# Optimization experiments

Measured on AMD Instinct MI355X. Metric: run time of the kernel, lower is better.

Reference implementation:

```python
import jax, jax.numpy as jnp
import numpy as np

EPS = 1e-06

def _feature_map(x):
    # elu_feature_map: phi(x) = elu(x) + 1  (strictly positive features)
    return jax.nn.elu(x) + 1.0

def setup_inputs() -> dict:
    key = jax.random.key(0)
    kq, kk, kv = jax.random.split(key, 3)
    N, L, H, D, M = 2, 2048, 8, 64, 64
    return {
        "queries": jax.random.normal(kq, (N, L, H, D), dtype=jnp.float32),
        "keys": jax.random.normal(kk, (N, L, H, D), dtype=jnp.float32),
        "values": jax.random.normal(kv, (N, L, H, M), dtype=jnp.float32),
    }

def reference(queries, keys, values):
    Q = _feature_map(queries)   # [N,L,H,D]
    K = _feature_map(keys)      # [N,L,H,D]
    # normalizer: Z_i = 1 / (Q_i . sum_{j<=i} K_j + eps)
    Z = 1.0 / (jnp.einsum('nlhi,nlhi->nlh', Q, jnp.cumsum(K, axis=1)) + EPS)
    # causal linear attention: S_i = sum_{j<=i} K_j outer V_j ; out_i = Q_i @ S_i
    S = jnp.cumsum(jnp.einsum('nlhd,nlhm->nlhdm', K, values), axis=1)  # [N,L,H,D,M]
    V = jnp.einsum('nlhd,nlhdm->nlhm', Q, S)
    return V * Z[:, :, :, None]
```

## Files before the change

### kernel.cpp

```cpp
#include <hip/hip_runtime.h>


namespace {
constexpr int N_ = 2, L_ = 2048, H_ = 8, D_ = 64, M_ = 64;
constexpr int C  = 64;
constexpr int G  = L_ / C;
constexpr int NH = N_ * H_;
constexpr int LDH = H_ * D_;
constexpr int TS  = 72;
constexpr float EPS_ = 1e-6f;
}

typedef __attribute__((ext_vector_type(8))) short short8;
typedef __attribute__((ext_vector_type(4))) float f32x4;

__device__ __forceinline__ float phi(float x) {
    return x > 0.0f ? x + 1.0f : __expf(x);
}
__device__ __forceinline__ unsigned short f2bf(float x) {
    unsigned int u = __float_as_uint(x);
    u += 0x7fffu + ((u >> 16) & 1u);
    return (unsigned short)(u >> 16);
}
__device__ __forceinline__ float bf2f(unsigned short h) {
    return __uint_as_float(((unsigned int)h) << 16);
}

__global__ __launch_bounds__(256, 4) void k_chunksum(
    const float* __restrict__ keys, const float* __restrict__ values,
    float* __restrict__ wsS, float* __restrict__ wsK)
{
    __shared__ __align__(16) unsigned short Kt[C * TS];
    __shared__ __align__(16) unsigned short Vt[C * TS];
    const int bid = blockIdx.x;
    const int g = bid % G, nh = bid / G;
    const int n = nh / H_, h = nh % H_;
    const int t = threadIdx.x;
    const size_t base = ((size_t)(n * L_ + g * C) * H_ + h) * D_;

#pragma unroll
    for (int r = 0; r < 4; ++r) {
        const int f = t + 256 * r;
        const int j = f >> 4, c = (f & 15) * 4;
        const size_t ga = base + (size_t)j * LDH + c;
        const float4 kv = *(const float4*)(keys + ga);
        const float4 vv = *(const float4*)(values + ga);
        Kt[(c + 0) * TS + j] = f2bf(phi(kv.x));
        Kt[(c + 1) * TS + j] = f2bf(phi(kv.y));
        Kt[(c + 2) * TS + j] = f2bf(phi(kv.z));
        Kt[(c + 3) * TS + j] = f2bf(phi(kv.w));
        Vt[(c + 0) * TS + j] = f2bf(vv.x);
        Vt[(c + 1) * TS + j] = f2bf(vv.y);
        Vt[(c + 2) * TS + j] = f2bf(vv.z);
        Vt[(c + 3) * TS + j] = f2bf(vv.w);
    }
    __syncthreads();

    const int w = t >> 6, lane = t & 63;
    const int row16 = lane & 15, quad = lane >> 4;

    f32x4 acc[4] = {f32x4{0,0,0,0}, f32x4{0,0,0,0}, f32x4{0,0,0,0}, f32x4{0,0,0,0}};
    f32x4 accK = f32x4{0,0,0,0};
    const unsigned short one_bf = 0x3F80;
    short8 ones;
#pragma unroll
    for (int i = 0; i < 8; ++i) ones[i] = (short)one_bf;

#pragma unroll
    for (int kt = 0; kt < 2; ++kt) {
        const short8 a = *(const short8*)&Kt[(16 * w + row16) * TS + quad * 8 + 32 * kt];
#pragma unroll
        for (int c = 0; c < 4; ++c) {
            const short8 b = *(const short8*)&Vt[(16 * c + row16) * TS + quad * 8 + 32 * kt];
            acc[c] = __builtin_amdgcn_mfma_f32_16x16x32_bf16(a, b, acc[c], 0, 0, 0);
        }
        accK = __builtin_amdgcn_mfma_f32_16x16x32_bf16(a, ones, accK, 0, 0, 0);
    }

    float* Sc = wsS + (size_t)bid * (D_ * M_);
#pragma unroll
    for (int c = 0; c < 4; ++c)
#pragma unroll
        for (int r = 0; r < 4; ++r)
            Sc[(16 * w + quad * 4 + r) * M_ + 16 * c + row16] = acc[c][r];

    if (row16 == 0) {
#pragma unroll
        for (int r = 0; r < 4; ++r)
            wsK[(size_t)bid * D_ + 16 * w + quad * 4 + r] = accK[r];
    }
}

__global__ __launch_bounds__(256) void k_scan(
    float* __restrict__ wsS, float* __restrict__ wsK)
{
    const int bid = blockIdx.x;
    const int nh = bid >> 4, q = bid & 15;
    const int t = threadIdx.x;

    float* base = wsS + (size_t)nh * G * (D_ * M_) + q * 256 + t;
    float run = 0.f;
#pragma unroll
    for (int g = 0; g < G; ++g) {
        float* p = base + (size_t)g * (D_ * M_);
        const float v = *p;
        *p = run;
        run += v;
    }

    if (q == 0 && t < D_) {
        float rk = 0.f;
        float* kb = wsK + (size_t)nh * G * D_ + t;
#pragma unroll
        for (int g = 0; g < G; ++g) {
            float* p = kb + (size_t)g * D_;
            const float v = *p;
            *p = rk;
            rk += v;
        }
    }
}

__global__ __launch_bounds__(256, 4) void k_out(
    const float* __restrict__ queries, const float* __restrict__ keys,
    const float* __restrict__ values, float* __restrict__ out,
    const float* __restrict__ wsS, const float* __restrict__ wsK)
{
    __shared__ __align__(16) unsigned short Qb[C * TS];
    __shared__ __align__(16) unsigned short Kb[C * TS];
    __shared__ __align__(16) unsigned short Vt[C * TS];
    __shared__ __align__(16) unsigned short St[C * TS];
    __shared__ float Rs[C];
    __shared__ float Zs[C];

    const int bid = blockIdx.x;
    const int g = bid % G, nh = bid / G;
    const int n = nh / H_, h = nh % H_;
    const int t = threadIdx.x;
    const size_t base = ((size_t)(n * L_ + g * C) * H_ + h) * D_;
    const float* Sp = wsS + (size_t)bid * (D_ * M_);
    const float* kpref = wsK + (size_t)bid * D_;

#pragma unroll
    for (int r = 0; r < 4; ++r) {
        const int f = t + 256 * r;
        const int row = f >> 4, c = (f & 15) * 4;
        const size_t ga = base + (size_t)row * LDH + c;
        const float4 qv = *(const float4*)(queries + ga);
        const float4 kv = *(const float4*)(keys + ga);
        const float4 vv = *(const float4*)(values + ga);
        Qb[row * TS + c + 0] = f2bf(phi(qv.x));
        Qb[row * TS + c + 1] = f2bf(phi(qv.y));
        Qb[row * TS + c + 2] = f2bf(phi(qv.z));
        Qb[row * TS + c + 3] = f2bf(phi(qv.w));
        Kb[row * TS + c + 0] = f2bf(phi(kv.x));
        Kb[row * TS + c + 1] = f2bf(phi(kv.y));
        Kb[row * TS + c + 2] = f2bf(phi(kv.z));
        Kb[row * TS + c + 3] = f2bf(phi(kv.w));
        Vt[(c + 0) * TS + row] = f2bf(vv.x);
        Vt[(c + 1) * TS + row] = f2bf(vv.y);
        Vt[(c + 2) * TS + row] = f2bf(vv.z);
        Vt[(c + 3) * TS + row] = f2bf(vv.w);
        const float4 sv = *(const float4*)(Sp + (size_t)row * M_ + c);
        St[(c + 0) * TS + row] = f2bf(sv.x);
        St[(c + 1) * TS + row] = f2bf(sv.y);
        St[(c + 2) * TS + row] = f2bf(sv.z);
        St[(c + 3) * TS + row] = f2bf(sv.w);
    }
    __syncthreads();

    const int w = t >> 6, lane = t & 63;
    const int row16 = lane & 15, quad = lane >> 4;

    short8 aq[2];
#pragma unroll
    for (int kt = 0; kt < 2; ++kt)
        aq[kt] = *(const short8*)&Qb[(16 * w + row16) * TS + quad * 8 + 32 * kt];

    f32x4 accA[4] = {f32x4{0,0,0,0}, f32x4{0,0,0,0}, f32x4{0,0,0,0}, f32x4{0,0,0,0}};
#pragma unroll
    for (int kt = 0; kt < 2; ++kt)
#pragma unroll
        for (int c = 0; c < 4; ++c) {
            const short8 b = *(const short8*)&Kb[(16 * c + row16) * TS + quad * 8 + 32 * kt];
            accA[c] = __builtin_amdgcn_mfma_f32_16x16x32_bf16(aq[kt], b, accA[c], 0, 0, 0);
        }

    float rs[4] = {0.f, 0.f, 0.f, 0.f};
#pragma unroll
    for (int c = 0; c < 4; ++c)
#pragma unroll
        for (int r = 0; r < 4; ++r) {
            const int row = 16 * w + quad * 4 + r;
            const int col = 16 * c + row16;
            const float v = (col <= row) ? accA[c][r] : 0.f;
            accA[c][r] = v;
            rs[r] += v;
        }
#pragma unroll
    for (int off = 1; off < 16; off <<= 1)
#pragma unroll
        for (int r = 0; r < 4; ++r)
            rs[r] += __shfl_xor(rs[r], off, 64);
    if (row16 == 0) {
#pragma unroll
        for (int r = 0; r < 4; ++r)
            Rs[16 * w + quad * 4 + r] = rs[r];
    }
    __syncthreads();

#pragma unroll
    for (int c = 0; c < 4; ++c)
#pragma unroll
        for (int r = 0; r < 4; ++r)
            Kb[(16 * w + quad * 4 + r) * TS + 16 * c + row16] = f2bf(accA[c][r]);

    if (t < C) {
        float zd = 0.f;
#pragma unroll 8
        for (int d = 0; d < D_; ++d)
            zd += bf2f(Qb[t * TS + d]) * kpref[d];
        Zs[t] = 1.0f / (zd + Rs[t] + EPS_);
    }
    __syncthreads();

    f32x4 accO[4] = {f32x4{0,0,0,0}, f32x4{0,0,0,0}, f32x4{0,0,0,0}, f32x4{0,0,0,0}};
#pragma unroll
    for (int kt = 0; kt < 2; ++kt) {
        const short8 aA = *(const short8*)&Kb[(16 * w + row16) * TS + quad * 8 + 32 * kt];
#pragma unroll
        for (int c = 0; c < 4; ++c) {
            const short8 bV = *(const short8*)&Vt[(16 * c + row16) * TS + quad * 8 + 32 * kt];
            accO[c] = __builtin_amdgcn_mfma_f32_16x16x32_bf16(aA, bV, accO[c], 0, 0, 0);
        }
#pragma unroll
        for (int c = 0; c < 4; ++c) {
            const short8 bS = *(const short8*)&St[(16 * c + row16) * TS + quad * 8 + 32 * kt];
            accO[c] = __builtin_amdgcn_mfma_f32_16x16x32_bf16(aq[kt], bS, accO[c], 0, 0, 0);
        }
    }

#pragma unroll
    for (int r = 0; r < 4; ++r) {
        const int row = 16 * w + quad * 4 + r;
        const float z = Zs[row];
        const size_t ob = ((size_t)(n * L_ + g * C + row) * H_ + h) * M_;
#pragma unroll
        for (int c = 0; c < 4; ++c)
            out[ob + 16 * c + row16] = accO[c][r] * z;
    }
}

extern "C" void kernel_launch(void* const* d_in, const int* in_sizes, int n_in,
                              void* d_out, int out_size, void* d_ws, size_t ws_size,
                              hipStream_t stream) {
    const float* q = (const float*)d_in[0];
    const float* k = (const float*)d_in[1];
    const float* v = (const float*)d_in[2];
    float* out = (float*)d_out;
    float* wsS = (float*)d_ws;
    float* wsK = wsS + (size_t)NH * G * D_ * M_;

    k_chunksum<<<dim3(NH * G), dim3(256), 0, stream>>>(k, v, wsS, wsK);
    k_scan<<<dim3(NH * 16), dim3(256), 0, stream>>>(wsS, wsK);
    k_out<<<dim3(NH * G), dim3(256), 0, stream>>>(q, k, v, out, wsS, wsK);
}
```

Before: 86.02 us.

## Store chunk state workspace as transposed bf16 to cut memory traffic

After: 84.67 us. No clear change (-1.6%).

```diff
diff --git a/kernel.cpp b/kernel.cpp
--- a/kernel.cpp
+++ b/kernel.cpp
@@ -28,7 +28,7 @@
 
 __global__ __launch_bounds__(256, 4) void k_chunksum(
     const float* __restrict__ keys, const float* __restrict__ values,
-    float* __restrict__ wsS, float* __restrict__ wsK)
+    unsigned short* __restrict__ wsSb, float* __restrict__ wsK)
 {
     __shared__ __align__(16) unsigned short Kt[C * TS];
     __shared__ __align__(16) unsigned short Vt[C * TS];
@@ -61,10 +61,9 @@
 
     f32x4 acc[4] = {f32x4{0,0,0,0}, f32x4{0,0,0,0}, f32x4{0,0,0,0}, f32x4{0,0,0,0}};
     f32x4 accK = f32x4{0,0,0,0};
-    const unsigned short one_bf = 0x3F80;
     short8 ones;
 #pragma unroll
-    for (int i = 0; i < 8; ++i) ones[i] = (short)one_bf;
+    for (int i = 0; i < 8; ++i) ones[i] = (short)0x3F80;
 
 #pragma unroll
     for (int kt = 0; kt < 2; ++kt) {
@@ -77,12 +76,14 @@
         accK = __builtin_amdgcn_mfma_f32_16x16x32_bf16(a, ones, accK, 0, 0, 0);
     }
 
-    float* Sc = wsS + (size_t)bid * (D_ * M_);
-#pragma unroll
-    for (int c = 0; c < 4; ++c)
-#pragma unroll
-        for (int r = 0; r < 4; ++r)
-            Sc[(16 * w + quad * 4 + r) * M_ + 16 * c + row16] = acc[c][r];
+    unsigned short* Sc = wsSb + (size_t)bid * (D_ * M_);
+#pragma unroll
+    for (int c = 0; c < 4; ++c) {
+        ushort4 pk;
+        pk.x = f2bf(acc[c][0]); pk.y = f2bf(acc[c][1]);
+        pk.z = f2bf(acc[c][2]); pk.w = f2bf(acc[c][3]);
+        *(ushort4*)(Sc + (16 * c + row16) * D_ + 16 * w + quad * 4) = pk;
+    }
 
     if (row16 == 0) {
 #pragma unroll
@@ -92,20 +93,23 @@
 }
 
 __global__ __launch_bounds__(256) void k_scan(
-    float* __restrict__ wsS, float* __restrict__ wsK)
+    unsigned short* __restrict__ wsSb, float* __restrict__ wsK)
 {
     const int bid = blockIdx.x;
-    const int nh = bid >> 4, q = bid & 15;
+    const int nh = bid >> 3, q = bid & 7;
     const int t = threadIdx.x;
 
-    float* base = wsS + (size_t)nh * G * (D_ * M_) + q * 256 + t;
-    float run = 0.f;
+    unsigned int* base =
+        (unsigned int*)(wsSb + (size_t)nh * G * (D_ * M_) + q * 512 + t * 2);
+    float r0 = 0.f, r1 = 0.f;
 #pragma unroll
     for (int g = 0; g < G; ++g) {
-        float* p = base + (size_t)g * (D_ * M_);
-        const float v = *p;
-        *p = run;
-        run += v;
+        unsigned int* p = base + (size_t)g * (D_ * M_ / 2);
+        const unsigned int v = *p;
+        const float v0 = bf2f((unsigned short)(v & 0xffffu));
+        const float v1 = bf2f((unsigned short)(v >> 16));
+        *p = ((unsigned int)f2bf(r1) << 16) | (unsigned int)f2bf(r0);
+        r0 += v0; r1 += v1;
     }
 
     if (q == 0 && t < D_) {
@@ -124,7 +128,7 @@
 __global__ __launch_bounds__(256, 4) void k_out(
     const float* __restrict__ queries, const float* __restrict__ keys,
     const float* __restrict__ values, float* __restrict__ out,
-    const float* __restrict__ wsS, const float* __restrict__ wsK)
+    const unsigned short* __restrict__ wsSb, const float* __restrict__ wsK)
 {
     __shared__ __align__(16) unsigned short Qb[C * TS];
     __shared__ __align__(16) unsigned short Kb[C * TS];
@@ -138,7 +142,7 @@
     const int n = nh / H_, h = nh % H_;
     const int t = threadIdx.x;
     const size_t base = ((size_t)(n * L_ + g * C) * H_ + h) * D_;
-    const float* Sp = wsS + (size_t)bid * (D_ * M_);
+    const unsigned short* Spb = wsSb + (size_t)bid * (D_ * M_);
     const float* kpref = wsK + (size_t)bid * D_;
 
 #pragma unroll
@@ -161,11 +165,12 @@
         Vt[(c + 1) * TS + row] = f2bf(vv.y);
         Vt[(c + 2) * TS + row] = f2bf(vv.z);
         Vt[(c + 3) * TS + row] = f2bf(vv.w);
-        const float4 sv = *(const float4*)(Sp + (size_t)row * M_ + c);
-        St[(c + 0) * TS + row] = f2bf(sv.x);
-        St[(c + 1) * TS + row] = f2bf(sv.y);
-        St[(c + 2) * TS + row] = f2bf(sv.z);
-        St[(c + 3) * TS + row] = f2bf(sv.w);
+    }
+#pragma unroll
+    for (int r = 0; r < 2; ++r) {
+        const int idx = t + 256 * r;
+        const int m = idx >> 3, dg = (idx & 7) * 8;
+        *(short8*)&St[m * TS + dg] = *(const short8*)(Spb + m * D_ + dg);
     }
     __syncthreads();
 
@@ -258,10 +263,10 @@
     const float* k = (const float*)d_in[1];
     const float* v = (const float*)d_in[2];
     float* out = (float*)d_out;
-    float* wsS = (float*)d_ws;
-    float* wsK = wsS + (size_t)NH * G * D_ * M_;
-
-    k_chunksum<<<dim3(NH * G), dim3(256), 0, stream>>>(k, v, wsS, wsK);
-    k_scan<<<dim3(NH * 16), dim3(256), 0, stream>>>(wsS, wsK);
-    k_out<<<dim3(NH * G), dim3(256), 0, stream>>>(q, k, v, out, wsS, wsK);
-}
+    unsigned short* wsSb = (unsigned short*)d_ws;
+    float* wsK = (float*)((char*)d_ws + (size_t)NH * G * D_ * M_ * 2);
+
+    k_chunksum<<<dim3(NH * G), dim3(256), 0, stream>>>(k, v, wsSb, wsK);
+    k_scan<<<dim3(NH * 8), dim3(256), 0, stream>>>(wsSb, wsK);
+    k_out<<<dim3(NH * G), dim3(256), 0, stream>>>(q, k, v, out, wsSb, wsK);
+}
```
